# Performance work log

Hardware: AMD Instinct MI355X
Metric: run time of the kernel (lower is better)

Reference implementation:

```python
import jax, jax.numpy as jnp
import numpy as np

D_MODEL = 1024
HEAD = 16
HEAD_DIM = D_MODEL // HEAD
BATCH = 2
SEQ = 2048


def setup_inputs() -> dict:
    key = jax.random.key(0)
    ks = jax.random.split(key, 11)
    s = 0.02
    return {
        "q": jax.random.normal(ks[0], (BATCH, SEQ, D_MODEL), dtype=jnp.float32),
        "k": jax.random.normal(ks[1], (BATCH, SEQ, D_MODEL), dtype=jnp.float32),
        "v": jax.random.normal(ks[2], (BATCH, SEQ, D_MODEL), dtype=jnp.float32),
        "w_q": jax.random.normal(ks[3], (D_MODEL, D_MODEL), dtype=jnp.float32) * s,
        "b_q": jnp.zeros((D_MODEL,), dtype=jnp.float32),
        "w_k": jax.random.normal(ks[4], (D_MODEL, D_MODEL), dtype=jnp.float32) * s,
        "b_k": jnp.zeros((D_MODEL,), dtype=jnp.float32),
        "w_v": jax.random.normal(ks[5], (D_MODEL, D_MODEL), dtype=jnp.float32) * s,
        "b_v": jnp.zeros((D_MODEL,), dtype=jnp.float32),
        "w_o": jax.random.normal(ks[6], (D_MODEL, D_MODEL), dtype=jnp.float32) * s,
        "b_o": jnp.zeros((D_MODEL,), dtype=jnp.float32),
    }


def reference(q, k, v, w_q, b_q, w_k, b_k, w_v, b_v, w_o, b_o):
    B, S, _ = q.shape
    # linear projections (torch Linear: x @ W^T + b)
    qp = q @ w_q.T + b_q
    kp = k @ w_k.T + b_k
    vp = v @ w_v.T + b_v
    # [B, S, H, Dh] -> [B, H, S, Dh]
    qh = qp.reshape(B, S, HEAD, HEAD_DIM).transpose(0, 2, 1, 3)
    kh = kp.reshape(B, S, HEAD, HEAD_DIM).transpose(0, 2, 1, 3)
    vh = vp.reshape(B, S, HEAD, HEAD_DIM).transpose(0, 2, 1, 3)
    # scaled dot-product attention with explicit score matrix
    scale = 1.0 / jnp.sqrt(jnp.float32(HEAD_DIM))
    scores = jnp.einsum("bhqd,bhkd->bhqk", qh, kh) * scale  # [B,H,S,S]
    attn = jax.nn.softmax(scores, axis=-1)
    z = jnp.einsum("bhqk,bhkd->bhqd", attn, vh)
    z = z.transpose(0, 2, 1, 3).reshape(B, S, D_MODEL)
    z = z @ w_o.T + b_o
    return (z, attn)
```

## Files before the change

### kernel.cpp

```cpp
#include <hip/hip_runtime.h>
#include <hip/hip_bf16.h>

#define D_MODEL 1024
#define NHEAD   16
#define HDIM    64
#define BATCH   2
#define SEQ     2048
#define BS_TOK  (BATCH*SEQ)

using bf16 = __hip_bfloat16;
typedef __attribute__((ext_vector_type(8))) short frag8;
typedef __attribute__((ext_vector_type(4))) float facc4;

__global__ __launch_bounds__(256) void cvt_f32_bf16(const float4* __restrict__ in,
                                                    ushort4* __restrict__ out, int n4) {
    int i = blockIdx.x * 256 + threadIdx.x;
    if (i >= n4) return;
    float4 v = in[i];
    bf16 a = __float2bfloat16(v.x), b = __float2bfloat16(v.y),
         c = __float2bfloat16(v.z), d = __float2bfloat16(v.w);
    ushort4 u;
    __builtin_memcpy(&u.x, &a, 2);
    __builtin_memcpy(&u.y, &b, 2);
    __builtin_memcpy(&u.z, &c, 2);
    __builtin_memcpy(&u.w, &d, 2);
    out[i] = u;
}

template<bool OUT_BF16, bool ROW_BIAS>
__global__ __launch_bounds__(256) void gemm_bt(const bf16* __restrict__ A,
                                               const bf16* __restrict__ Bt,
                                               const float* __restrict__ bias,
                                               void* __restrict__ Cout,
                                               int M, int N, int K) {
    __shared__ bf16 As[64][40];
    __shared__ bf16 Bs[64][40];
    const int tid  = threadIdx.x;
    const int lane = tid & 63, wave = tid >> 6;
    const int wm = wave >> 1, wn = wave & 1;
    const int L15 = lane & 15, quad = lane >> 4;
    const int m0 = blockIdx.y * 64, n0 = blockIdx.x * 64;
    const int lr = tid >> 2;
    const int lc = (tid & 3) * 8;

    const facc4 zero4 = {0.f, 0.f, 0.f, 0.f};
    facc4 acc[2][2];
    acc[0][0] = zero4; acc[0][1] = zero4; acc[1][0] = zero4; acc[1][1] = zero4;

    for (int k0 = 0; k0 < K; k0 += 32) {
        uint4 av = *(const uint4*)(A  + (size_t)(m0 + lr) * K + k0 + lc);
        uint4 bv = *(const uint4*)(Bt + (size_t)(n0 + lr) * K + k0 + lc);
        *(uint4*)&As[lr][lc] = av;
        *(uint4*)&Bs[lr][lc] = bv;
        __syncthreads();
        frag8 a0 = *(const frag8*)&As[wm * 32 +  0 + L15][quad * 8];
        frag8 a1 = *(const frag8*)&As[wm * 32 + 16 + L15][quad * 8];
        frag8 b0 = *(const frag8*)&Bs[wn * 32 +  0 + L15][quad * 8];
        frag8 b1 = *(const frag8*)&Bs[wn * 32 + 16 + L15][quad * 8];
        acc[0][0] = __builtin_amdgcn_mfma_f32_16x16x32_bf16(a0, b0, acc[0][0], 0, 0, 0);
        acc[0][1] = __builtin_amdgcn_mfma_f32_16x16x32_bf16(a0, b1, acc[0][1], 0, 0, 0);
        acc[1][0] = __builtin_amdgcn_mfma_f32_16x16x32_bf16(a1, b0, acc[1][0], 0, 0, 0);
        acc[1][1] = __builtin_amdgcn_mfma_f32_16x16x32_bf16(a1, b1, acc[1][1], 0, 0, 0);
        __syncthreads();
    }
#pragma unroll
    for (int mt = 0; mt < 2; mt++)
#pragma unroll
        for (int nt = 0; nt < 2; nt++)
#pragma unroll
            for (int r = 0; r < 4; r++) {
                int row = m0 + wm * 32 + mt * 16 + quad * 4 + r;
                int col = n0 + wn * 32 + nt * 16 + L15;
                float v = acc[mt][nt][r] + (ROW_BIAS ? bias[row] : bias[col]);
                if (OUT_BF16) ((bf16*)Cout)[(size_t)row * N + col] = __float2bfloat16(v);
                else          ((float*)Cout)[(size_t)row * N + col] = v;
            }
}

__device__ __forceinline__ int pidx(int row, int col) {
    int chunk = col >> 3;
    return row * 2048 + (((chunk ^ (row & 7)) << 3) | (col & 7));
}

__global__ __launch_bounds__(256) void attn_kernel(const bf16* __restrict__ qp,
                                                   const bf16* __restrict__ kp,
                                                   const bf16* __restrict__ vT,
                                                   bf16* __restrict__ zbuf,
                                                   float* __restrict__ attn_out,
                                                   float* __restrict__ redg,
                                                   float* __restrict__ invg) {
    __shared__ bf16 pbuf[16 * 2048];
    const int bid = blockIdx.x;
    const int strip = bid & 127, bh = bid >> 7;
    const int b = bh >> 4, h = bh & 15;
    const int i0 = strip * 16;
    const int tid = threadIdx.x, lane = tid & 63, wave = tid >> 6;
    const int L15 = lane & 15, quad = lane >> 4;
    const float scale = 0.125f;

    frag8 aq0, aq1;
    {
        size_t base = (size_t)(b * SEQ + i0 + L15) * D_MODEL + h * HDIM + quad * 8;
        aq0 = *(const frag8*)(qp + base);
        aq1 = *(const frag8*)(qp + base + 32);
    }

    const facc4 zero4 = {0.f, 0.f, 0.f, 0.f};
    float sums[4] = {0.f, 0.f, 0.f, 0.f};

    for (int tt = 0; tt < 32; tt++) {
        int j0 = (wave + tt * 4) * 16;
        size_t kb = (size_t)(b * SEQ + j0 + L15) * D_MODEL + h * HDIM + quad * 8;
        frag8 kb0 = *(const frag8*)(kp + kb);
        frag8 kb1 = *(const frag8*)(kp + kb + 32);
        facc4 acc = zero4;
        acc = __builtin_amdgcn_mfma_f32_16x16x32_bf16(aq0, kb0, acc, 0, 0, 0);
        acc = __builtin_amdgcn_mfma_f32_16x16x32_bf16(aq1, kb1, acc, 0, 0, 0);
        int col = j0 + L15;
#pragma unroll
        for (int r = 0; r < 4; r++) {
            int row = quad * 4 + r;
            float p = __expf(acc[r] * scale);
            sums[r] += p;
            pbuf[pidx(row, col)] = __float2bfloat16(p);
        }
    }
#pragma unroll
    for (int m = 1; m <= 8; m <<= 1)
#pragma unroll
        for (int r = 0; r < 4; r++) sums[r] += __shfl_xor(sums[r], m, 64);
    if (L15 == 0) {
#pragma unroll
        for (int r = 0; r < 4; r++)
            redg[((size_t)bid * 4 + wave) * 16 + quad * 4 + r] = sums[r];
    }
    __syncthreads();
    if (tid < 16) {
        float s = 0.f;
#pragma unroll
        for (int w = 0; w < 4; w++) s += redg[((size_t)bid * 4 + w) * 16 + tid];
        invg[(size_t)bid * 16 + tid] = 1.0f / s;
    }
    __syncthreads();

    {
        facc4 accz = zero4;
        const int d = wave * 16 + L15;
        const bf16* vrow = vT + (size_t)(h * HDIM + d) * BS_TOK + b * SEQ;
        for (int k0 = 0; k0 < SEQ; k0 += 32) {
            int chunk = (k0 >> 3) + quad;
            frag8 pa = *(const frag8*)&pbuf[L15 * 2048 + ((chunk ^ (L15 & 7)) << 3)];
            frag8 vb = *(const frag8*)(vrow + k0 + quad * 8);
            accz = __builtin_amdgcn_mfma_f32_16x16x32_bf16(pa, vb, accz, 0, 0, 0);
        }
#pragma unroll
        for (int r = 0; r < 4; r++) {
            int i = quad * 4 + r;
            float inv = invg[(size_t)bid * 16 + i];
            size_t row = (size_t)(b * SEQ + i0 + i);
            zbuf[row * D_MODEL + h * HDIM + d] = __float2bfloat16(accz[r] * inv);
        }
    }

    {
        size_t obase = ((size_t)bh * SEQ + i0) * SEQ;
        for (int e = tid; e < 16 * 512; e += 256) {
            int i = e >> 9;
            int c0 = (e & 511) << 2;
            float inv = invg[(size_t)bid * 16 + i];
            const bf16* src = &pbuf[pidx(i, c0)];
            float4 o = make_float4(__bfloat162float(src[0]) * inv,
                                   __bfloat162float(src[1]) * inv,
                                   __bfloat162float(src[2]) * inv,
                                   __bfloat162float(src[3]) * inv);
            *(float4*)(attn_out + obase + (size_t)i * SEQ + c0) = o;
        }
    }
}

extern "C" void kernel_launch(void* const* d_in, const int* in_sizes, int n_in,
                              void* d_out, int out_size, void* d_ws, size_t ws_size,
                              hipStream_t stream) {
    const float* q   = (const float*)d_in[0];
    const float* k   = (const float*)d_in[1];
    const float* v   = (const float*)d_in[2];
    const float* w_q = (const float*)d_in[3];
    const float* b_q = (const float*)d_in[4];
    const float* w_k = (const float*)d_in[5];
    const float* b_k = (const float*)d_in[6];
    const float* w_v = (const float*)d_in[7];
    const float* b_v = (const float*)d_in[8];
    const float* w_o = (const float*)d_in[9];
    const float* b_o = (const float*)d_in[10];

    char* ws = (char*)d_ws;
    const size_t TOK = (size_t)BS_TOK * D_MODEL;
    const size_t WM  = (size_t)D_MODEL * D_MODEL;
    bf16* qbf  = (bf16*)(ws);
    bf16* kbf  = (bf16*)(ws + 8388608);
    bf16* vbf  = (bf16*)(ws + 16777216);
    bf16* wqb  = (bf16*)(ws + 25165824);
    bf16* wkb  = (bf16*)(ws + 27262976);
    bf16* wvb  = (bf16*)(ws + 29360128);
    bf16* wob  = (bf16*)(ws + 31457280);
    bf16* qp   = (bf16*)(ws + 33554432);
    bf16* kp   = (bf16*)(ws + 41943040);
    bf16* vT   = (bf16*)(ws + 50331648);
    bf16* zbf  = (bf16*)(ws + 58720256);
    float* redg = (float*)(ws + 67108864);
    float* invg = (float*)(ws + 68157440);

    float* z_out    = (float*)d_out;
    float* attn_out = (float*)d_out + (size_t)BATCH * SEQ * D_MODEL;

    int n4t = (int)(TOK / 4), n4w = (int)(WM / 4);
    cvt_f32_bf16<<<(n4t + 255) / 256, 256, 0, stream>>>((const float4*)q, (ushort4*)qbf, n4t);
    cvt_f32_bf16<<<(n4t + 255) / 256, 256, 0, stream>>>((const float4*)k, (ushort4*)kbf, n4t);
    cvt_f32_bf16<<<(n4t + 255) / 256, 256, 0, stream>>>((const float4*)v, (ushort4*)vbf, n4t);
    cvt_f32_bf16<<<(n4w + 255) / 256, 256, 0, stream>>>((const float4*)w_q, (ushort4*)wqb, n4w);
    cvt_f32_bf16<<<(n4w + 255) / 256, 256, 0, stream>>>((const float4*)w_k, (ushort4*)wkb, n4w);
    cvt_f32_bf16<<<(n4w + 255) / 256, 256, 0, stream>>>((const float4*)w_v, (ushort4*)wvb, n4w);
    cvt_f32_bf16<<<(n4w + 255) / 256, 256, 0, stream>>>((const float4*)w_o, (ushort4*)wob, n4w);

    dim3 g1(D_MODEL / 64, BS_TOK / 64);
    gemm_bt<true, false><<<g1, 256, 0, stream>>>(qbf, wqb, b_q, qp, BS_TOK, D_MODEL, D_MODEL);
    gemm_bt<true, false><<<g1, 256, 0, stream>>>(kbf, wkb, b_k, kp, BS_TOK, D_MODEL, D_MODEL);
    dim3 g2(BS_TOK / 64, D_MODEL / 64);
    gemm_bt<true, true><<<g2, 256, 0, stream>>>(wvb, vbf, b_v, vT, D_MODEL, BS_TOK, D_MODEL);

    attn_kernel<<<BATCH * NHEAD * (SEQ / 16), 256, 0, stream>>>(qp, kp, vT, zbf, attn_out,
                                                                redg, invg);

    gemm_bt<false, false><<<g1, 256, 0, stream>>>(zbf, wob, b_o, z_out, BS_TOK, D_MODEL, D_MODEL);
}
```

Before: 964.4 us.

## Recompute scores in chunks, fuse attn output writes, enlarge GEMM tiles with direct LDS loads

The attention kernel now computes row sums in a first pass and recomputes QK^T in a second pass over 512-column chunks. That pass writes normalized probabilities straight to global memory with nontemporal stores and accumulates PV from a small LDS tile. This shrinks LDS use from 64KB to about 16KB, which should raise occupancy, and removes the global scratch reductions, at the cost of computing QK^T twice. The GEMM moves to 128x64 tiles loaded with global_load_lds, and the seven conversion launches are merged into two. The unpadded 32-wide LDS rows may cause bank conflicts when fragments are read.

Result: no change. 955.0 us (-1.0%).

```diff
diff --git a/kernel.cpp b/kernel.cpp
--- a/kernel.cpp
+++ b/kernel.cpp
@@ -1,5 +1,6 @@
 #include <hip/hip_runtime.h>
 #include <hip/hip_bf16.h>
+#include <stdint.h>
 
 #define D_MODEL 1024
 #define NHEAD   16
@@ -12,19 +13,34 @@
 typedef __attribute__((ext_vector_type(8))) short frag8;
 typedef __attribute__((ext_vector_type(4))) float facc4;
 
-__global__ __launch_bounds__(256) void cvt_f32_bf16(const float4* __restrict__ in,
-                                                    ushort4* __restrict__ out, int n4) {
-    int i = blockIdx.x * 256 + threadIdx.x;
+__device__ __forceinline__ void gld_lds16(const void* g, void* l) {
+    __builtin_amdgcn_global_load_lds(
+        reinterpret_cast<const __attribute__((address_space(1))) uint32_t*>(
+            reinterpret_cast<uintptr_t>(g)),
+        reinterpret_cast<__attribute__((address_space(3))) uint32_t*>(
+            reinterpret_cast<uintptr_t>(l)),
+        16, 0, 0);
+}
+
+__global__ __launch_bounds__(256) void cvt_multi(const float4* __restrict__ s0, const float4* __restrict__ s1,
+                                                 const float4* __restrict__ s2, const float4* __restrict__ s3,
+                                                 ushort4* __restrict__ d0, ushort4* __restrict__ d1,
+                                                 ushort4* __restrict__ d2, ushort4* __restrict__ d3,
+                                                 int n4, int nblk) {
+    int t = blockIdx.x / nblk;
+    int i = (blockIdx.x - t * nblk) * 256 + threadIdx.x;
     if (i >= n4) return;
-    float4 v = in[i];
+    const float4* s = (t == 0) ? s0 : (t == 1) ? s1 : (t == 2) ? s2 : s3;
+    ushort4*       d = (t == 0) ? d0 : (t == 1) ? d1 : (t == 2) ? d2 : d3;
+    float4 v = s[i];
     bf16 a = __float2bfloat16(v.x), b = __float2bfloat16(v.y),
-         c = __float2bfloat16(v.z), d = __float2bfloat16(v.w);
+         c = __float2bfloat16(v.z), e = __float2bfloat16(v.w);
     ushort4 u;
     __builtin_memcpy(&u.x, &a, 2);
     __builtin_memcpy(&u.y, &b, 2);
     __builtin_memcpy(&u.z, &c, 2);
-    __builtin_memcpy(&u.w, &d, 2);
-    out[i] = u;
+    __builtin_memcpy(&u.w, &e, 2);
+    d[i] = u;
 }
 
 template<bool OUT_BF16, bool ROW_BIAS>
@@ -33,43 +49,54 @@
                                                const float* __restrict__ bias,
                                                void* __restrict__ Cout,
                                                int M, int N, int K) {
-    __shared__ bf16 As[64][40];
-    __shared__ bf16 Bs[64][40];
+    __shared__ bf16 As[128 * 32];
+    __shared__ bf16 Bs[64 * 32];
     const int tid  = threadIdx.x;
     const int lane = tid & 63, wave = tid >> 6;
     const int wm = wave >> 1, wn = wave & 1;
     const int L15 = lane & 15, quad = lane >> 4;
-    const int m0 = blockIdx.y * 64, n0 = blockIdx.x * 64;
-    const int lr = tid >> 2;
-    const int lc = (tid & 3) * 8;
+    const int m0 = blockIdx.y * 128, n0 = blockIdx.x * 64;
+    const int r1 = tid >> 2;
+    const int c1 = (tid & 3) * 8;
+
+    const bf16* Ag0 = A  + (size_t)(m0 +      r1) * K + c1;
+    const bf16* Ag1 = A  + (size_t)(m0 + 64 + r1) * K + c1;
+    const bf16* Bg0 = Bt + (size_t)(n0 +      r1) * K + c1;
+    bf16* As0 = As + wave * 512;
+    bf16* As1 = As + 2048 + wave * 512;
+    bf16* Bs0 = Bs + wave * 512;
 
     const facc4 zero4 = {0.f, 0.f, 0.f, 0.f};
-    facc4 acc[2][2];
-    acc[0][0] = zero4; acc[0][1] = zero4; acc[1][0] = zero4; acc[1][1] = zero4;
+    facc4 acc[4][2];
+#pragma unroll
+    for (int mt = 0; mt < 4; mt++) { acc[mt][0] = zero4; acc[mt][1] = zero4; }
 
     for (int k0 = 0; k0 < K; k0 += 32) {
-        uint4 av = *(const uint4*)(A  + (size_t)(m0 + lr) * K + k0 + lc);
-        uint4 bv = *(const uint4*)(Bt + (size_t)(n0 + lr) * K + k0 + lc);
-        *(uint4*)&As[lr][lc] = av;
-        *(uint4*)&Bs[lr][lc] = bv;
-        __syncthreads();
-        frag8 a0 = *(const frag8*)&As[wm * 32 +  0 + L15][quad * 8];
-        frag8 a1 = *(const frag8*)&As[wm * 32 + 16 + L15][quad * 8];
-        frag8 b0 = *(const frag8*)&Bs[wn * 32 +  0 + L15][quad * 8];
-        frag8 b1 = *(const frag8*)&Bs[wn * 32 + 16 + L15][quad * 8];
-        acc[0][0] = __builtin_amdgcn_mfma_f32_16x16x32_bf16(a0, b0, acc[0][0], 0, 0, 0);
-        acc[0][1] = __builtin_amdgcn_mfma_f32_16x16x32_bf16(a0, b1, acc[0][1], 0, 0, 0);
-        acc[1][0] = __builtin_amdgcn_mfma_f32_16x16x32_bf16(a1, b0, acc[1][0], 0, 0, 0);
-        acc[1][1] = __builtin_amdgcn_mfma_f32_16x16x32_bf16(a1, b1, acc[1][1], 0, 0, 0);
-        __syncthreads();
-    }
-#pragma unroll
-    for (int mt = 0; mt < 2; mt++)
+        gld_lds16(Ag0 + k0, As0);
+        gld_lds16(Ag1 + k0, As1);
+        gld_lds16(Bg0 + k0, Bs0);
+        __syncthreads();
+        frag8 af[4], bfr[2];
+#pragma unroll
+        for (int mt = 0; mt < 4; mt++)
+            af[mt] = *(const frag8*)&As[(wm * 64 + mt * 16 + L15) * 32 + quad * 8];
 #pragma unroll
         for (int nt = 0; nt < 2; nt++)
+            bfr[nt] = *(const frag8*)&Bs[(wn * 32 + nt * 16 + L15) * 32 + quad * 8];
+#pragma unroll
+        for (int mt = 0; mt < 4; mt++)
+#pragma unroll
+            for (int nt = 0; nt < 2; nt++)
+                acc[mt][nt] = __builtin_amdgcn_mfma_f32_16x16x32_bf16(af[mt], bfr[nt], acc[mt][nt], 0, 0, 0);
+        __syncthreads();
+    }
+#pragma unroll
+    for (int mt = 0; mt < 4; mt++)
+#pragma unroll
+        for (int nt = 0; nt < 2; nt++)
 #pragma unroll
             for (int r = 0; r < 4; r++) {
-                int row = m0 + wm * 32 + mt * 16 + quad * 4 + r;
+                int row = m0 + wm * 64 + mt * 16 + quad * 4 + r;
                 int col = n0 + wn * 32 + nt * 16 + L15;
                 float v = acc[mt][nt][r] + (ROW_BIAS ? bias[row] : bias[col]);
                 if (OUT_BF16) ((bf16*)Cout)[(size_t)row * N + col] = __float2bfloat16(v);
@@ -77,19 +104,19 @@
             }
 }
 
-__device__ __forceinline__ int pidx(int row, int col) {
+__device__ __forceinline__ int pidx2(int row, int col) {
     int chunk = col >> 3;
-    return row * 2048 + (((chunk ^ (row & 7)) << 3) | (col & 7));
+    return row * 512 + (((chunk ^ (row & 7)) << 3) | (col & 7));
 }
 
 __global__ __launch_bounds__(256) void attn_kernel(const bf16* __restrict__ qp,
                                                    const bf16* __restrict__ kp,
                                                    const bf16* __restrict__ vT,
                                                    bf16* __restrict__ zbuf,
-                                                   float* __restrict__ attn_out,
-                                                   float* __restrict__ redg,
-                                                   float* __restrict__ invg) {
-    __shared__ bf16 pbuf[16 * 2048];
+                                                   float* __restrict__ attn_out) {
+    __shared__ bf16 ptile[16 * 512];
+    __shared__ float sred[4][16];
+    __shared__ float sinv[16];
     const int bid = blockIdx.x;
     const int strip = bid & 127, bh = bid >> 7;
     const int b = bh >> 4, h = bh & 15;
@@ -104,26 +131,19 @@
         aq0 = *(const frag8*)(qp + base);
         aq1 = *(const frag8*)(qp + base + 32);
     }
-
     const facc4 zero4 = {0.f, 0.f, 0.f, 0.f};
+
     float sums[4] = {0.f, 0.f, 0.f, 0.f};
-
     for (int tt = 0; tt < 32; tt++) {
-        int j0 = (wave + tt * 4) * 16;
+        int j0 = wave * 512 + tt * 16;
         size_t kb = (size_t)(b * SEQ + j0 + L15) * D_MODEL + h * HDIM + quad * 8;
-        frag8 kb0 = *(const frag8*)(kp + kb);
-        frag8 kb1 = *(const frag8*)(kp + kb + 32);
+        frag8 kf0 = *(const frag8*)(kp + kb);
+        frag8 kf1 = *(const frag8*)(kp + kb + 32);
         facc4 acc = zero4;
-        acc = __builtin_amdgcn_mfma_f32_16x16x32_bf16(aq0, kb0, acc, 0, 0, 0);
-        acc = __builtin_amdgcn_mfma_f32_16x16x32_bf16(aq1, kb1, acc, 0, 0, 0);
-        int col = j0 + L15;
-#pragma unroll
-        for (int r = 0; r < 4; r++) {
-            int row = quad * 4 + r;
-            float p = __expf(acc[r] * scale);
-            sums[r] += p;
-            pbuf[pidx(row, col)] = __float2bfloat16(p);
-        }
+        acc = __builtin_amdgcn_mfma_f32_16x16x32_bf16(aq0, kf0, acc, 0, 0, 0);
+        acc = __builtin_amdgcn_mfma_f32_16x16x32_bf16(aq1, kf1, acc, 0, 0, 0);
+#pragma unroll
+        for (int r = 0; r < 4; r++) sums[r] += __expf(acc[r] * scale);
     }
 #pragma unroll
     for (int m = 1; m <= 8; m <<= 1)
@@ -131,50 +151,52 @@
         for (int r = 0; r < 4; r++) sums[r] += __shfl_xor(sums[r], m, 64);
     if (L15 == 0) {
 #pragma unroll
-        for (int r = 0; r < 4; r++)
-            redg[((size_t)bid * 4 + wave) * 16 + quad * 4 + r] = sums[r];
+        for (int r = 0; r < 4; r++) sred[wave][quad * 4 + r] = sums[r];
     }
     __syncthreads();
-    if (tid < 16) {
-        float s = 0.f;
-#pragma unroll
-        for (int w = 0; w < 4; w++) s += redg[((size_t)bid * 4 + w) * 16 + tid];
-        invg[(size_t)bid * 16 + tid] = 1.0f / s;
-    }
+    if (tid < 16) sinv[tid] = 1.0f / (sred[0][tid] + sred[1][tid] + sred[2][tid] + sred[3][tid]);
     __syncthreads();
 
-    {
-        facc4 accz = zero4;
-        const int d = wave * 16 + L15;
-        const bf16* vrow = vT + (size_t)(h * HDIM + d) * BS_TOK + b * SEQ;
-        for (int k0 = 0; k0 < SEQ; k0 += 32) {
-            int chunk = (k0 >> 3) + quad;
-            frag8 pa = *(const frag8*)&pbuf[L15 * 2048 + ((chunk ^ (L15 & 7)) << 3)];
-            frag8 vb = *(const frag8*)(vrow + k0 + quad * 8);
-            accz = __builtin_amdgcn_mfma_f32_16x16x32_bf16(pa, vb, accz, 0, 0, 0);
+    float invr[4];
+#pragma unroll
+    for (int r = 0; r < 4; r++) invr[r] = sinv[quad * 4 + r];
+
+    facc4 zacc = zero4;
+    const bf16* vrow = vT + (size_t)(h * HDIM + wave * 16 + L15) * BS_TOK + b * SEQ;
+    const size_t obase = ((size_t)bh * SEQ + i0) * SEQ;
+
+    for (int c = 0; c < 4; c++) {
+        for (int tt = 0; tt < 8; tt++) {
+            int jrel = wave * 128 + tt * 16;
+            int j0 = c * 512 + jrel;
+            size_t kb = (size_t)(b * SEQ + j0 + L15) * D_MODEL + h * HDIM + quad * 8;
+            frag8 kf0 = *(const frag8*)(kp + kb);
+            frag8 kf1 = *(const frag8*)(kp + kb + 32);
+            facc4 acc = zero4;
+            acc = __builtin_amdgcn_mfma_f32_16x16x32_bf16(aq0, kf0, acc, 0, 0, 0);
+            acc = __builtin_amdgcn_mfma_f32_16x16x32_bf16(aq1, kf1, acc, 0, 0, 0);
+            int colw = jrel + L15;
+#pragma unroll
+            for (int r = 0; r < 4; r++) {
+                int row = quad * 4 + r;
+                float a = __expf(acc[r] * scale) * invr[r];
+                __builtin_nontemporal_store(a, attn_out + obase + (size_t)row * SEQ + j0 + L15);
+                ptile[pidx2(row, colw)] = __float2bfloat16(a);
+            }
         }
-#pragma unroll
-        for (int r = 0; r < 4; r++) {
-            int i = quad * 4 + r;
-            float inv = invg[(size_t)bid * 16 + i];
-            size_t row = (size_t)(b * SEQ + i0 + i);
-            zbuf[row * D_MODEL + h * HDIM + d] = __float2bfloat16(accz[r] * inv);
+        __syncthreads();
+#pragma unroll 4
+        for (int k0 = 0; k0 < 512; k0 += 32) {
+            frag8 pa = *(const frag8*)&ptile[L15 * 512 + ((((k0 >> 3) + quad) ^ (L15 & 7)) << 3)];
+            frag8 vb = *(const frag8*)(vrow + c * 512 + k0 + quad * 8);
+            zacc = __builtin_amdgcn_mfma_f32_16x16x32_bf16(pa, vb, zacc, 0, 0, 0);
         }
-    }
-
-    {
-        size_t obase = ((size_t)bh * SEQ + i0) * SEQ;
-        for (int e = tid; e < 16 * 512; e += 256) {
-            int i = e >> 9;
-            int c0 = (e & 511) << 2;
-            float inv = invg[(size_t)bid * 16 + i];
-            const bf16* src = &pbuf[pidx(i, c0)];
-            float4 o = make_float4(__bfloat162float(src[0]) * inv,
-                                   __bfloat162float(src[1]) * inv,
-                                   __bfloat162float(src[2]) * inv,
-                                   __bfloat162float(src[3]) * inv);
-            *(float4*)(attn_out + obase + (size_t)i * SEQ + c0) = o;
-        }
+        __syncthreads();
+    }
+#pragma unroll
+    for (int r = 0; r < 4; r++) {
+        size_t row = (size_t)(b * SEQ + i0 + quad * 4 + r);
+        zbuf[row * D_MODEL + h * HDIM + wave * 16 + L15] = __float2bfloat16(zacc[r]);
     }
 }
 
@@ -207,29 +229,28 @@
     bf16* kp   = (bf16*)(ws + 41943040);
     bf16* vT   = (bf16*)(ws + 50331648);
     bf16* zbf  = (bf16*)(ws + 58720256);
-    float* redg = (float*)(ws + 67108864);
-    float* invg = (float*)(ws + 68157440);
 
     float* z_out    = (float*)d_out;
     float* attn_out = (float*)d_out + (size_t)BATCH * SEQ * D_MODEL;
 
     int n4t = (int)(TOK / 4), n4w = (int)(WM / 4);
-    cvt_f32_bf16<<<(n4t + 255) / 256, 256, 0, stream>>>((const float4*)q, (ushort4*)qbf, n4t);
-    cvt_f32_bf16<<<(n4t + 255) / 256, 256, 0, stream>>>((const float4*)k, (ushort4*)kbf, n4t);
-    cvt_f32_bf16<<<(n4t + 255) / 256, 256, 0, stream>>>((const float4*)v, (ushort4*)vbf, n4t);
-    cvt_f32_bf16<<<(n4w + 255) / 256, 256, 0, stream>>>((const float4*)w_q, (ushort4*)wqb, n4w);
-    cvt_f32_bf16<<<(n4w + 255) / 256, 256, 0, stream>>>((const float4*)w_k, (ushort4*)wkb, n4w);
-    cvt_f32_bf16<<<(n4w + 255) / 256, 256, 0, stream>>>((const float4*)w_v, (ushort4*)wvb, n4w);
-    cvt_f32_bf16<<<(n4w + 255) / 256, 256, 0, stream>>>((const float4*)w_o, (ushort4*)wob, n4w);
-
-    dim3 g1(D_MODEL / 64, BS_TOK / 64);
+    int nbt = (n4t + 255) / 256, nbw = (n4w + 255) / 256;
+    cvt_multi<<<3 * nbt, 256, 0, stream>>>((const float4*)q, (const float4*)k, (const float4*)v,
+                                           (const float4*)v,
+                                           (ushort4*)qbf, (ushort4*)kbf, (ushort4*)vbf,
+                                           (ushort4*)vbf, n4t, nbt);
+    cvt_multi<<<4 * nbw, 256, 0, stream>>>((const float4*)w_q, (const float4*)w_k,
+                                           (const float4*)w_v, (const float4*)w_o,
+                                           (ushort4*)wqb, (ushort4*)wkb, (ushort4*)wvb,
+                                           (ushort4*)wob, n4w, nbw);
+
+    dim3 g1(D_MODEL / 64, BS_TOK / 128);
     gemm_bt<true, false><<<g1, 256, 0, stream>>>(qbf, wqb, b_q, qp, BS_TOK, D_MODEL, D_MODEL);
     gemm_bt<true, false><<<g1, 256, 0, stream>>>(kbf, wkb, b_k, kp, BS_TOK, D_MODEL, D_MODEL);
-    dim3 g2(BS_TOK / 64, D_MODEL / 64);
+    dim3 g2(BS_TOK / 64, D_MODEL / 128);
     gemm_bt<true, true><<<g2, 256, 0, stream>>>(wvb, vbf, b_v, vT, D_MODEL, BS_TOK, D_MODEL);
 
-    attn_kernel<<<BATCH * NHEAD * (SEQ / 16), 256, 0, stream>>>(qp, kp, vT, zbf, attn_out,
-                                                                redg, invg);
+    attn_kernel<<<BATCH * NHEAD * (SEQ / 16), 256, 0, stream>>>(qp, kp, vT, zbf, attn_out);
 
     gemm_bt<false, false><<<g1, 256, 0, stream>>>(zbf, wob, b_o, z_out, BS_TOK, D_MODEL, D_MODEL);
 }
```
